# Kernel optimization log

Measured on AMD Instinct MI355X. Metric: run time of the kernel, lower is better.

The kernel has to match this reference:

```python
import jax, jax.numpy as jnp
import numpy as np

B, S, D, H = 2, 2048, 1024, 16
DH = D // H  # 64


def setup_inputs() -> dict:
    key = jax.random.key(0)
    ks = jax.random.split(key, 10)
    inp = {
        "q": jax.random.normal(ks[0], (B, S, D), jnp.float32),
        "k": jax.random.normal(ks[1], (B, S, D), jnp.float32),
        "v": jax.random.normal(ks[2], (B, S, D), jnp.float32),
        "mask": jax.random.randint(ks[3], (B, S), 0, 2, jnp.int32),
        "Wq": jax.random.normal(ks[4], (D, D), jnp.float32) * 0.02,
        "bq": jnp.zeros((D,), jnp.float32),
        "Wk": jax.random.normal(ks[5], (D, D), jnp.float32) * 0.02,
        "bk": jnp.zeros((D,), jnp.float32),
        "Wv": jax.random.normal(ks[6], (D, D), jnp.float32) * 0.02,
        "bv": jnp.zeros((D,), jnp.float32),
    }
    return inp


def _split_heads(x):
    # [B, S, D] -> [B, H, S, DH]
    b, s, _ = x.shape
    return x.reshape(b, s, H, DH).transpose(0, 2, 1, 3)


def reference(q, k, v, mask, Wq, bq, Wk, bk, Wv, bv):
    qh = _split_heads(q @ Wq + bq)
    kh = _split_heads(k @ Wk + bk)
    vh = _split_heads(v @ Wv + bv)
    # NOTE: original scales by sqrt(hidden_size), not sqrt(head_dim)
    scores = jnp.einsum("bhqd,bhkd->bhqk", qh, kh) / jnp.sqrt(jnp.float32(D))
    m = mask.astype(jnp.float32)[:, None, None, :]  # [B,1,1,S_k]
    scores = scores + (-1e9) * (1.0 - m)
    weights = jax.nn.softmax(scores, axis=-1)
    out = jnp.einsum("bhqk,bhkd->bhqd", weights, vh)
    # concat heads: [B,H,S,DH] -> [B,S,D]
    return out.transpose(0, 2, 1, 3).reshape(q.shape[0], -1, D)
```

## Files before the change

kernel.cpp:

```cpp
#include <hip/hip_runtime.h>


#define B_ 2
#define S_ 2048
#define D_ 1024
#define H_ 16
#define DH_ 64
#define M_ (B_*S_)

#define WT_OFF  ((size_t)3*4194304)
#define XB_OFF  (WT_OFF + (size_t)3*1048576)

typedef __attribute__((ext_vector_type(8))) short short8;
typedef __attribute__((ext_vector_type(4))) float f32x4;
#define MFMA16(a,b,c) __builtin_amdgcn_mfma_f32_16x16x32_bf16(a,b,c,0,0,0)

typedef __attribute__((address_space(1))) const void* gptr_t;
typedef __attribute__((address_space(3))) void* lptr_t;
static __device__ inline void gload_lds16(const void* g, void* l) {
    __builtin_amdgcn_global_load_lds((gptr_t)g, (lptr_t)l, 16, 0, 0);
}

static __device__ inline unsigned short f2bf(float x) {
    union { float f; unsigned u; } v; v.f = x;
    return (unsigned short)((v.u + 0x7fffu + ((v.u >> 16) & 1u)) >> 16);
}
static __device__ inline unsigned packp(float a, float b) {
    return __builtin_amdgcn_perm(__float_as_uint(b) + 0x8000u,
                                 __float_as_uint(a) + 0x8000u, 0x07060302u);
}

__global__ __launch_bounds__(256) void convert_x3(
    const float* __restrict__ X0, const float* __restrict__ X1,
    const float* __restrict__ X2, unsigned short* __restrict__ O0,
    unsigned short* __restrict__ O1, unsigned short* __restrict__ O2)
{
    const int z = blockIdx.z;
    const float* X = z==0 ? X0 : (z==1 ? X1 : X2);
    unsigned short* O = z==0 ? O0 : (z==1 ? O1 : O2);
    int idx = blockIdx.x*256 + threadIdx.x;
    float4 xv = *(const float4*)&X[(size_t)idx*4];
    uint2 o;
    o.x = (unsigned)f2bf(xv.x) | ((unsigned)f2bf(xv.y) << 16);
    o.y = (unsigned)f2bf(xv.z) | ((unsigned)f2bf(xv.w) << 16);
    *(uint2*)&O[(size_t)idx*4] = o;
}

__global__ __launch_bounds__(256) void convert_w(
    const float* __restrict__ Wq, const float* __restrict__ Wk,
    const float* __restrict__ Wv, unsigned short* __restrict__ WtBase)
{
    const int which = blockIdx.z;
    const float* W = which==0 ? Wq : (which==1 ? Wk : Wv);
    unsigned short* Out = WtBase + ((size_t)which << 20);

    __shared__ unsigned short T[64][72];
    const int t  = threadIdx.x;
    const int n0 = blockIdx.x*64, k0 = blockIdx.y*64;
    const int tk = t >> 4, tn4 = (t & 15)*4;

    #pragma unroll
    for (int i=0;i<4;i++){
        int kk = tk + i*16;
        float4 wv = *(const float4*)&W[(size_t)(k0+kk)*D_ + n0 + tn4];
        T[tn4+0][kk] = f2bf(wv.x);
        T[tn4+1][kk] = f2bf(wv.y);
        T[tn4+2][kk] = f2bf(wv.z);
        T[tn4+3][kk] = f2bf(wv.w);
    }
    __syncthreads();

    const int n = t >> 2, seg = t & 3;
    uint4 a = *(uint4*)&T[n][seg*16];
    uint4 b = *(uint4*)&T[n][seg*16 + 8];
    *(uint4*)&Out[(size_t)(n0+n)*D_ + k0 + seg*16]     = a;
    *(uint4*)&Out[(size_t)(n0+n)*D_ + k0 + seg*16 + 8] = b;
}

__global__ __launch_bounds__(256) void proj_gemm(
    const unsigned short* __restrict__ A0, const unsigned short* __restrict__ A1,
    const unsigned short* __restrict__ A2, const unsigned short* __restrict__ WtBase,
    const float* __restrict__ b0, const float* __restrict__ b1,
    const float* __restrict__ b2, unsigned short* __restrict__ OutBase)
{
    const int which = blockIdx.z;
    const unsigned short* A  = which==0 ? A0 : (which==1 ? A1 : A2);
    const unsigned short* Bm = WtBase + ((size_t)which << 20);
    const float* bias        = which==0 ? b0 : (which==1 ? b1 : b2);
    unsigned short* Out      = OutBase + ((size_t)which << 22);
    const float oscale = (which==0) ? 0.04508422f : 1.0f;

    __shared__ __align__(16) unsigned short As[128*64];
    __shared__ __align__(16) unsigned short Bs[128*64];

    const int t    = threadIdx.x;
    const int m0   = blockIdx.y * 128;
    const int n0   = blockIdx.x * 128;
    const int w    = t >> 6;
    const int lane = t & 63;
    const int l15  = lane & 15;
    const int quad = lane >> 4;
    const int wm   = w >> 1, wn = w & 1;

    f32x4 acc[4][4];
    #pragma unroll
    for (int i=0;i<4;i++)
        #pragma unroll
        for (int j=0;j<4;j++) acc[i][j] = (f32x4){0.f,0.f,0.f,0.f};

    float biasv[4];
    #pragma unroll
    for (int nt=0; nt<4; nt++)
        biasv[nt] = bias[n0 + wn*64 + nt*16 + l15];

    int sArow[4], sAkc[4];
    #pragma unroll
    for (int i=0;i<4;i++){
        int s  = (w*4 + i)*64 + lane;
        int r  = s >> 3, cs = s & 7;
        sArow[i] = r;
        sAkc[i]  = ((cs ^ (r & 7)) * 8);
    }

    for (int ks = 0; ks < 16; ++ks) {
        const int kb = ks * 64;
        #pragma unroll
        for (int i=0;i<4;i++){
            int s = (w*4 + i)*64 + lane;
            gload_lds16(A  + (size_t)(m0 + sArow[i])*D_ + kb + sAkc[i], (unsigned short*)As + s*8);
            gload_lds16(Bm + (size_t)(n0 + sArow[i])*D_ + kb + sAkc[i], (unsigned short*)Bs + s*8);
        }
        __syncthreads();

        #pragma unroll
        for (int kh=0; kh<2; kh++){
            short8 aF[4], bF[4];
            #pragma unroll
            for (int mt=0; mt<4; mt++){
                int r  = wm*64 + mt*16 + l15;
                int cs = (kh*4 + quad) ^ (r & 7);
                aF[mt] = *(const short8*)(As + r*64 + cs*8);
            }
            #pragma unroll
            for (int nt=0; nt<4; nt++){
                int r  = wn*64 + nt*16 + l15;
                int cs = (kh*4 + quad) ^ (r & 7);
                bF[nt] = *(const short8*)(Bs + r*64 + cs*8);
            }
            #pragma unroll
            for (int mt=0; mt<4; mt++)
                #pragma unroll
                for (int nt=0; nt<4; nt++)
                    acc[mt][nt] = MFMA16(aF[mt], bF[nt], acc[mt][nt]);
        }
        __syncthreads();
    }

    if (which != 2) {
        #pragma unroll
        for (int nt=0; nt<4; nt++){
            int n  = n0 + wn*64 + nt*16 + l15;
            int hh = n >> 6, dh = n & 63;
            #pragma unroll
            for (int mt=0; mt<4; mt++){
                #pragma unroll
                for (int r=0; r<4; r++){
                    int m  = m0 + wm*64 + mt*16 + quad*4 + r;
                    int bb = m >> 11, ss = m & (S_-1);
                    float v = (acc[mt][nt][r] + biasv[nt]) * oscale;
                    Out[((size_t)((bb*H_ + hh)*S_ + ss))*DH_ + dh] = f2bf(v);
                }
            }
        }
    } else {
        #pragma unroll
        for (int nt=0; nt<4; nt++){
            int n  = n0 + wn*64 + nt*16 + l15;
            int hh = n >> 6, dh = n & 63;
            #pragma unroll
            for (int mt=0; mt<4; mt++){
                int m  = m0 + wm*64 + mt*16 + quad*4;
                int bb = m >> 11, ss = m & (S_-1);
                uint2 pk;
                pk.x = packp(acc[mt][nt][0] + biasv[nt], acc[mt][nt][1] + biasv[nt]);
                pk.y = packp(acc[mt][nt][2] + biasv[nt], acc[mt][nt][3] + biasv[nt]);
                *(uint2*)&Out[((size_t)((bb*H_ + hh)*DH_ + dh))*S_ + ss] = pk;
            }
        }
    }
}

__global__ __launch_bounds__(256) void attn_kernel(
    const unsigned short* __restrict__ ws, const int* __restrict__ mask,
    float* __restrict__ out)
{
    const unsigned short* Qh = ws;
    const unsigned short* Kh = ws + (size_t)M_*D_;
    const unsigned short* Vg = ws + 2*(size_t)M_*D_;

    const int qt = blockIdx.x;
    const int h  = blockIdx.y;
    const int bb = blockIdx.z;
    const size_t base = ((size_t)(bb*H_ + h)) * S_ * DH_;
    const int q0 = qt * 128;

    __shared__ __align__(16) unsigned char smem[51712];
    unsigned short* KsB = (unsigned short*)smem;
    unsigned short* VtB = (unsigned short*)(smem + 16384);
    unsigned short* Pb  = (unsigned short*)(smem + 32768);
    float*          MsB = (float*)(smem + 51200);
    float*          Ob  = (float*)smem;

    const int t    = threadIdx.x;
    const int w    = t >> 6;
    const int lane = t & 63;
    const int l15  = lane & 15;
    const int quad = lane >> 4;

    short8 qf[2][2];
    #pragma unroll
    for (int qs=0; qs<2; qs++){
        const unsigned short* qp = Qh + base + (size_t)(q0 + w*32 + qs*16 + l15)*DH_ + quad*8;
        qf[qs][0] = *(const short8*)(qp);
        qf[qs][1] = *(const short8*)(qp + 32);
    }

    f32x4 accO[2][4];
    #pragma unroll
    for (int qs=0; qs<2; qs++)
        #pragma unroll
        for (int i=0;i<4;i++) accO[qs][i] = (f32x4){0.f,0.f,0.f,0.f};
    float l_run[2] = {0.f, 0.f};

    int rr[2], cc[2], ssl[2];
    #pragma unroll
    for (int i=0;i<2;i++){
        int s = (w*2 + i)*64 + lane;
        ssl[i] = s;
        rr[i]  = s >> 3;
        cc[i]  = ((s & 7) ^ (rr[i] & 7)) * 8;
    }

    #define ISSUE(k0v, p) do {                                                 \
        _Pragma("unroll")                                                      \
        for (int i=0;i<2;i++){                                                 \
            gload_lds16(Kh + base + (size_t)((k0v) + rr[i])*DH_ + cc[i],       \
                        KsB + (p)*4096 + ssl[i]*8);                            \
            gload_lds16(Vg + base + (size_t)rr[i]*S_ + (k0v) + cc[i],          \
                        VtB + (p)*4096 + ssl[i]*8);                            \
        }                                                                      \
    } while(0)

    ISSUE(0, 0);
    if (t < 64) MsB[t] = mask[bb*S_ + t] ? 0.f : -1e9f;
    __syncthreads();

    for (int it = 0; it < 32; ++it){
        const int p = it & 1;
        int mR = 0;
        if (it < 31){
            ISSUE((it+1)*64, 1-p);
            if (t < 64) mR = mask[bb*S_ + (it+1)*64 + t];
        }
        const unsigned short* Ks  = KsB + p*4096;
        const unsigned short* Vts = VtB + p*4096;
        const float* Ms = MsB + p*64;

        f32x4 msv[4];
        #pragma unroll
        for (int st=0; st<4; st++)
            msv[st] = *(const f32x4*)&Ms[st*16 + quad*4];

        f32x4 sc[2][4];
        #pragma unroll
        for (int st=0; st<4; st++){
            int key = st*16 + l15;
            const unsigned short* kr = Ks + key*64;
            short8 ka = *(const short8*)(kr + ((quad    ) ^ (key & 7))*8);
            short8 kb = *(const short8*)(kr + ((quad + 4) ^ (key & 7))*8);
            #pragma unroll
            for (int qs=0; qs<2; qs++){
                f32x4 a = (f32x4){0.f,0.f,0.f,0.f};
                a = MFMA16(ka, qf[qs][0], a);
                a = MFMA16(kb, qf[qs][1], a);
                sc[qs][st] = a;
            }
        }

        #pragma unroll
        for (int qs=0; qs<2; qs++){
            float lacc = 0.f;
            unsigned short* pr = Pb + (w*32 + qs*16 + l15)*72;
            #pragma unroll
            for (int st=0; st<4; st++){
                float pv[4];
                #pragma unroll
                for (int r=0; r<4; r++){
                    pv[r] = __builtin_amdgcn_exp2f(sc[qs][st][r] + msv[st][r]);
                    lacc += pv[r];
                }
                uint2 pk;
                pk.x = packp(pv[0], pv[1]);
                pk.y = packp(pv[2], pv[3]);
                *(uint2*)(pr + st*16 + quad*4) = pk;
            }
            l_run[qs] += lacc;
        }

        short8 vf[4][2];
        #pragma unroll
        for (int mt=0; mt<4; mt++){
            int row = mt*16 + l15;
            const unsigned short* vr = Vts + row*64;
            vf[mt][0] = *(const short8*)(vr + ((quad    ) ^ (row & 7))*8);
            vf[mt][1] = *(const short8*)(vr + ((quad + 4) ^ (row & 7))*8);
        }
        #pragma unroll
        for (int qs=0; qs<2; qs++){
            const unsigned short* pr = Pb + (w*32 + qs*16 + l15)*72;
            short8 pf0 = *(const short8*)(pr + quad*8);
            short8 pf1 = *(const short8*)(pr + 32 + quad*8);
            #pragma unroll
            for (int mt=0; mt<4; mt++){
                accO[qs][mt] = MFMA16(vf[mt][0], pf0, accO[qs][mt]);
                accO[qs][mt] = MFMA16(vf[mt][1], pf1, accO[qs][mt]);
            }
        }

        if (it < 31 && t < 64) MsB[(1-p)*64 + t] = mR ? 0.f : -1e9f;
        __syncthreads();
    }

    #pragma unroll
    for (int qs=0; qs<2; qs++){
        float l = l_run[qs];
        l += __shfl_xor(l, 16);
        l += __shfl_xor(l, 32);
        float invl = 1.0f / fmaxf(l, 1e-30f);
        #pragma unroll
        for (int mt=0; mt<4; mt++)
            #pragma unroll
            for (int r=0; r<4; r++)
                Ob[(w*32 + qs*16 + l15)*68 + mt*16 + quad*4 + r] = accO[qs][mt][r]*invl;
    }
    __syncthreads();

    #pragma unroll
    for (int i=0;i<8;i++){
        int f  = (i*256 + t)*4;
        int qq = f >> 6, dh = f & 63;
        float4 o = *(float4*)&Ob[qq*68 + dh];
        *(float4*)&out[((size_t)(bb*S_ + q0 + qq))*D_ + h*DH_ + dh] = o;
    }
    #undef ISSUE
}

extern "C" void kernel_launch(void* const* d_in, const int* in_sizes, int n_in,
                              void* d_out, int out_size, void* d_ws, size_t ws_size,
                              hipStream_t stream) {
    const float* q    = (const float*)d_in[0];
    const float* k    = (const float*)d_in[1];
    const float* v    = (const float*)d_in[2];
    const int*   mask = (const int*)d_in[3];
    const float* Wq   = (const float*)d_in[4];
    const float* b0   = (const float*)d_in[5];
    const float* Wk   = (const float*)d_in[6];
    const float* b1   = (const float*)d_in[7];
    const float* Wv   = (const float*)d_in[8];
    const float* b2   = (const float*)d_in[9];
    float* out = (float*)d_out;
    unsigned short* ws = (unsigned short*)d_ws;

    unsigned short* xq = ws + XB_OFF;
    unsigned short* xk = (unsigned short*)d_out;
    unsigned short* xv = (unsigned short*)d_out + 4194304;

    convert_w<<<dim3(16,16,3), 256, 0, stream>>>(Wq, Wk, Wv, ws + WT_OFF);
    convert_x3<<<dim3(4096,1,3), 256, 0, stream>>>(q, k, v, xq, xk, xv);
    proj_gemm<<<dim3(8,32,3), 256, 0, stream>>>(xq, xk, xv, ws + WT_OFF,
                                                b0, b1, b2, ws);
    attn_kernel<<<dim3(16,16,2), 256, 0, stream>>>(ws, mask, out);
}
```

Before: 216.5 us.

## Halve attention query tile, fuse conversion kernels, and mask via select

The attention kernel now gives each block 64 query rows instead of 128, doubling the grid, and sets a launch bound of 4 blocks per CU. It also reads the mask directly from global memory and zeroes probabilities with a select instead of staging an additive bias in LDS, and swizzles the P buffer so it no longer needs padding. The weight and input conversion kernels are merged into one launch. The intent is higher occupancy and fewer launches, at the cost of reloading K/V tiles twice as often across blocks and doing redundant mask loads per lane. Prep launches 4096 blocks in the weight slice, and most of them exit early.

```diff
diff --git a/kernel.cpp b/kernel.cpp
--- a/kernel.cpp
+++ b/kernel.cpp
@@ -30,33 +30,36 @@
                                  __float_as_uint(a) + 0x8000u, 0x07060302u);
 }
 
-__global__ __launch_bounds__(256) void convert_x3(
+__global__ __launch_bounds__(256) void prep(
     const float* __restrict__ X0, const float* __restrict__ X1,
-    const float* __restrict__ X2, unsigned short* __restrict__ O0,
-    unsigned short* __restrict__ O1, unsigned short* __restrict__ O2)
+    const float* __restrict__ X2,
+    const float* __restrict__ Wq, const float* __restrict__ Wk,
+    const float* __restrict__ Wv,
+    unsigned short* __restrict__ O0, unsigned short* __restrict__ O1,
+    unsigned short* __restrict__ O2, unsigned short* __restrict__ WtBase)
 {
     const int z = blockIdx.z;
-    const float* X = z==0 ? X0 : (z==1 ? X1 : X2);
-    unsigned short* O = z==0 ? O0 : (z==1 ? O1 : O2);
-    int idx = blockIdx.x*256 + threadIdx.x;
-    float4 xv = *(const float4*)&X[(size_t)idx*4];
-    uint2 o;
-    o.x = (unsigned)f2bf(xv.x) | ((unsigned)f2bf(xv.y) << 16);
-    o.y = (unsigned)f2bf(xv.z) | ((unsigned)f2bf(xv.w) << 16);
-    *(uint2*)&O[(size_t)idx*4] = o;
-}
-
-__global__ __launch_bounds__(256) void convert_w(
-    const float* __restrict__ Wq, const float* __restrict__ Wk,
-    const float* __restrict__ Wv, unsigned short* __restrict__ WtBase)
-{
-    const int which = blockIdx.z;
+    const int t = threadIdx.x;
+    if (z < 3) {
+        const float* X = z==0 ? X0 : (z==1 ? X1 : X2);
+        unsigned short* O = z==0 ? O0 : (z==1 ? O1 : O2);
+        int idx = blockIdx.x*256 + t;
+        float4 xv = *(const float4*)&X[(size_t)idx*4];
+        uint2 o;
+        o.x = (unsigned)f2bf(xv.x) | ((unsigned)f2bf(xv.y) << 16);
+        o.y = (unsigned)f2bf(xv.z) | ((unsigned)f2bf(xv.w) << 16);
+        *(uint2*)&O[(size_t)idx*4] = o;
+        return;
+    }
+    const int bx = blockIdx.x;
+    if (bx >= 768) return;
+    const int which = bx >> 8;
+    const int tile  = bx & 255;
     const float* W = which==0 ? Wq : (which==1 ? Wk : Wv);
     unsigned short* Out = WtBase + ((size_t)which << 20);
 
     __shared__ unsigned short T[64][72];
-    const int t  = threadIdx.x;
-    const int n0 = blockIdx.x*64, k0 = blockIdx.y*64;
+    const int n0 = (tile & 15)*64, k0 = (tile >> 4)*64;
     const int tk = t >> 4, tn4 = (t & 15)*4;
 
     #pragma unroll
@@ -190,7 +193,7 @@
     }
 }
 
-__global__ __launch_bounds__(256) void attn_kernel(
+__global__ __launch_bounds__(256,4) void attn_kernel(
     const unsigned short* __restrict__ ws, const int* __restrict__ mask,
     float* __restrict__ out)
 {
@@ -202,13 +205,12 @@
     const int h  = blockIdx.y;
     const int bb = blockIdx.z;
     const size_t base = ((size_t)(bb*H_ + h)) * S_ * DH_;
-    const int q0 = qt * 128;
-
-    __shared__ __align__(16) unsigned char smem[51712];
+    const int q0 = qt * 64;
+
+    __shared__ __align__(16) unsigned char smem[40960];
     unsigned short* KsB = (unsigned short*)smem;
     unsigned short* VtB = (unsigned short*)(smem + 16384);
     unsigned short* Pb  = (unsigned short*)(smem + 32768);
-    float*          MsB = (float*)(smem + 51200);
     float*          Ob  = (float*)smem;
 
     const int t    = threadIdx.x;
@@ -216,21 +218,19 @@
     const int lane = t & 63;
     const int l15  = lane & 15;
     const int quad = lane >> 4;
-
-    short8 qf[2][2];
-    #pragma unroll
-    for (int qs=0; qs<2; qs++){
-        const unsigned short* qp = Qh + base + (size_t)(q0 + w*32 + qs*16 + l15)*DH_ + quad*8;
-        qf[qs][0] = *(const short8*)(qp);
-        qf[qs][1] = *(const short8*)(qp + 32);
-    }
-
-    f32x4 accO[2][4];
-    #pragma unroll
-    for (int qs=0; qs<2; qs++)
-        #pragma unroll
-        for (int i=0;i<4;i++) accO[qs][i] = (f32x4){0.f,0.f,0.f,0.f};
-    float l_run[2] = {0.f, 0.f};
+    const int sw   = l15 & 7;
+
+    short8 qf0, qf1;
+    {
+        const unsigned short* qp = Qh + base + (size_t)(q0 + w*16 + l15)*DH_ + quad*8;
+        qf0 = *(const short8*)(qp);
+        qf1 = *(const short8*)(qp + 32);
+    }
+
+    f32x4 accO[4];
+    #pragma unroll
+    for (int i=0;i<4;i++) accO[i] = (f32x4){0.f,0.f,0.f,0.f};
+    float l_run = 0.f;
 
     int rr[2], cc[2], ssl[2];
     #pragma unroll
@@ -252,101 +252,78 @@
     } while(0)
 
     ISSUE(0, 0);
-    if (t < 64) MsB[t] = mask[bb*S_ + t] ? 0.f : -1e9f;
     __syncthreads();
 
     for (int it = 0; it < 32; ++it){
         const int p = it & 1;
-        int mR = 0;
-        if (it < 31){
-            ISSUE((it+1)*64, 1-p);
-            if (t < 64) mR = mask[bb*S_ + (it+1)*64 + t];
-        }
+        if (it < 31) ISSUE((it+1)*64, 1-p);
+
+        int4 mk[4];
+        #pragma unroll
+        for (int st=0; st<4; st++)
+            mk[st] = *(const int4*)&mask[bb*S_ + it*64 + st*16 + quad*4];
+
         const unsigned short* Ks  = KsB + p*4096;
         const unsigned short* Vts = VtB + p*4096;
-        const float* Ms = MsB + p*64;
-
-        f32x4 msv[4];
-        #pragma unroll
-        for (int st=0; st<4; st++)
-            msv[st] = *(const f32x4*)&Ms[st*16 + quad*4];
-
-        f32x4 sc[2][4];
+
+        f32x4 sc[4];
         #pragma unroll
         for (int st=0; st<4; st++){
             int key = st*16 + l15;
             const unsigned short* kr = Ks + key*64;
             short8 ka = *(const short8*)(kr + ((quad    ) ^ (key & 7))*8);
             short8 kb = *(const short8*)(kr + ((quad + 4) ^ (key & 7))*8);
-            #pragma unroll
-            for (int qs=0; qs<2; qs++){
-                f32x4 a = (f32x4){0.f,0.f,0.f,0.f};
-                a = MFMA16(ka, qf[qs][0], a);
-                a = MFMA16(kb, qf[qs][1], a);
-                sc[qs][st] = a;
-            }
-        }
-
-        #pragma unroll
-        for (int qs=0; qs<2; qs++){
-            float lacc = 0.f;
-            unsigned short* pr = Pb + (w*32 + qs*16 + l15)*72;
-            #pragma unroll
-            for (int st=0; st<4; st++){
-                float pv[4];
-                #pragma unroll
-                for (int r=0; r<4; r++){
-                    pv[r] = __builtin_amdgcn_exp2f(sc[qs][st][r] + msv[st][r]);
-                    lacc += pv[r];
-                }
-                uint2 pk;
-                pk.x = packp(pv[0], pv[1]);
-                pk.y = packp(pv[2], pv[3]);
-                *(uint2*)(pr + st*16 + quad*4) = pk;
-            }
-            l_run[qs] += lacc;
-        }
-
-        short8 vf[4][2];
+            f32x4 a = (f32x4){0.f,0.f,0.f,0.f};
+            a = MFMA16(ka, qf0, a);
+            a = MFMA16(kb, qf1, a);
+            sc[st] = a;
+        }
+
+        float lacc = 0.f;
+        unsigned short* pr = Pb + (w*16 + l15)*64;
+        #pragma unroll
+        for (int st=0; st<4; st++){
+            float pv[4];
+            pv[0] = mk[st].x ? __builtin_amdgcn_exp2f(sc[st][0]) : 0.f;
+            pv[1] = mk[st].y ? __builtin_amdgcn_exp2f(sc[st][1]) : 0.f;
+            pv[2] = mk[st].z ? __builtin_amdgcn_exp2f(sc[st][2]) : 0.f;
+            pv[3] = mk[st].w ? __builtin_amdgcn_exp2f(sc[st][3]) : 0.f;
+            lacc += pv[0] + pv[1] + pv[2] + pv[3];
+            uint2 pk;
+            pk.x = packp(pv[0], pv[1]);
+            pk.y = packp(pv[2], pv[3]);
+            *(uint2*)(pr + (((st*2 + (quad>>1)) ^ sw)*8 + (quad&1)*4)) = pk;
+        }
+        l_run += lacc;
+
+        short8 pf0 = *(const short8*)(pr + ((quad    ) ^ sw)*8);
+        short8 pf1 = *(const short8*)(pr + ((quad + 4) ^ sw)*8);
         #pragma unroll
         for (int mt=0; mt<4; mt++){
             int row = mt*16 + l15;
             const unsigned short* vr = Vts + row*64;
-            vf[mt][0] = *(const short8*)(vr + ((quad    ) ^ (row & 7))*8);
-            vf[mt][1] = *(const short8*)(vr + ((quad + 4) ^ (row & 7))*8);
-        }
-        #pragma unroll
-        for (int qs=0; qs<2; qs++){
-            const unsigned short* pr = Pb + (w*32 + qs*16 + l15)*72;
-            short8 pf0 = *(const short8*)(pr + quad*8);
-            short8 pf1 = *(const short8*)(pr + 32 + quad*8);
-            #pragma unroll
-            for (int mt=0; mt<4; mt++){
-                accO[qs][mt] = MFMA16(vf[mt][0], pf0, accO[qs][mt]);
-                accO[qs][mt] = MFMA16(vf[mt][1], pf1, accO[qs][mt]);
-            }
-        }
-
-        if (it < 31 && t < 64) MsB[(1-p)*64 + t] = mR ? 0.f : -1e9f;
+            short8 vf0 = *(const short8*)(vr + ((quad    ) ^ (row & 7))*8);
+            short8 vf1 = *(const short8*)(vr + ((quad + 4) ^ (row & 7))*8);
+            accO[mt] = MFMA16(vf0, pf0, accO[mt]);
+            accO[mt] = MFMA16(vf1, pf1, accO[mt]);
+        }
+
         __syncthreads();
     }
 
-    #pragma unroll
-    for (int qs=0; qs<2; qs++){
-        float l = l_run[qs];
-        l += __shfl_xor(l, 16);
-        l += __shfl_xor(l, 32);
-        float invl = 1.0f / fmaxf(l, 1e-30f);
-        #pragma unroll
-        for (int mt=0; mt<4; mt++)
-            #pragma unroll
-            for (int r=0; r<4; r++)
-                Ob[(w*32 + qs*16 + l15)*68 + mt*16 + quad*4 + r] = accO[qs][mt][r]*invl;
-    }
+    float l = l_run;
+    l += __shfl_xor(l, 16);
+    l += __shfl_xor(l, 32);
+    float invl = 1.0f / fmaxf(l, 1e-30f);
+    #pragma unroll
+    for (int mt=0; mt<4; mt++)
+        #pragma unroll
+        for (int r=0; r<4; r++)
+            Ob[(w*16 + l15)*68 + mt*16 + quad*4 + r] = accO[mt][r]*invl;
     __syncthreads();
 
     #pragma unroll
-    for (int i=0;i<8;i++){
+    for (int i=0;i<4;i++){
         int f  = (i*256 + t)*4;
         int qq = f >> 6, dh = f & 63;
         float4 o = *(float4*)&Ob[qq*68 + dh];
@@ -375,9 +352,9 @@
     unsigned short* xk = (unsigned short*)d_out;
     unsigned short* xv = (unsigned short*)d_out + 4194304;
 
-    convert_w<<<dim3(16,16,3), 256, 0, stream>>>(Wq, Wk, Wv, ws + WT_OFF);
-    convert_x3<<<dim3(4096,1,3), 256, 0, stream>>>(q, k, v, xq, xk, xv);
+    prep<<<dim3(4096,1,4), 256, 0, stream>>>(q, k, v, Wq, Wk, Wv,
+                                             xq, xk, xv, ws + WT_OFF);
     proj_gemm<<<dim3(8,32,3), 256, 0, stream>>>(xq, xk, xv, ws + WT_OFF,
                                                 b0, b1, b2, ws);
-    attn_kernel<<<dim3(16,16,2), 256, 0, stream>>>(ws, mask, out);
-}
+    attn_kernel<<<dim3(32,16,2), 256, 0, stream>>>(ws, mask, out);
+}
```

Result: no change. 219.2 us (+1.2%).
